# Optimization experiments

Hardware: AMD Instinct MI355X
Metric: run time of the kernel (lower is better)

The kernel has to match this reference:

```python
import jax, jax.numpy as jnp
import numpy as np

RES = (64, 128, 256)          # res_plane per scale
CDIM = (32, 32, 32)           # plane_feat_dim per scale
PADDING = 0.1
EPS = 1e-5                    # torch code uses 10e-6
PLANE_AXES = {"xz": (0, 2), "xy": (0, 1), "yz": (1, 2)}


def _plane_features(coord, feats, plane, res):
    """coord: (B,N,3) float, feats: (B,N,C) float -> (B,C,res,res).
    Faithful to normalize_coordinate + coordinate2index + scatter_mean."""
    a, b = PLANE_AXES[plane]
    xy = jnp.stack([coord[..., a], coord[..., b]], axis=-1)   # (B,N,2)
    xy = xy / (1.0 + PADDING + EPS) + 0.5
    xy = jnp.clip(xy, 0.0, 1.0 - EPS)
    ij = (xy * res).astype(jnp.int32)                         # trunc == floor (nonneg)
    idx = ij[..., 0] + res * ij[..., 1]                       # (B,N) flattened grid index
    r2 = res * res

    def per_batch(f, i):  # f: (N,C), i: (N,)
        s = jax.ops.segment_sum(f, i, num_segments=r2)        # (R2,C) scatter-add
        c = jax.ops.segment_sum(jnp.ones((f.shape[0],), f.dtype), i, num_segments=r2)
        return s / jnp.maximum(c, 1.0)[:, None]               # scatter_mean: div by clamp(count,1)

    out = jax.vmap(per_batch)(feats, idx)                     # (B,R2,C)
    B, _, C = out.shape
    return out.transpose(0, 2, 1).reshape(B, C, res, res)


def _forward(f_list, c_list):
    # returns tuple over 3 scales, each a tuple (xz, xy, yz) of (B,C,res,res)
    return tuple(
        tuple(_plane_features(c, f, pl, r) for pl in ("xz", "xy", "yz"))
        for f, c, r in zip(f_list, c_list, RES)
    )


def setup_inputs() -> dict:
    key = jax.random.key(0)
    ks = jax.random.split(key, 6)
    B = 8
    Ns = (65536, 32768, 16384)
    inp = {}
    for i, (n, c) in enumerate(zip(Ns, CDIM)):
        inp[f"f{i}"] = jax.random.normal(ks[i], (B, n, c), dtype=jnp.float32)
        # coords in [-0.5, 0.5): normalize maps them into [0,1) grid range
        inp[f"c{i}"] = jax.random.uniform(ks[3 + i], (B, n, 3), dtype=jnp.float32) - 0.5
    return inp


def reference(f0, f1, f2, c0, c1, c2):
    return _forward((f0, f1, f2), (c0, c1, c2))
```

## Files before the change

### kernel.cpp

```cpp
#include <hip/hip_runtime.h>

static constexpr int B = 8;
static constexpr int C = 32;

typedef float vfloat4 __attribute__((ext_vector_type(4)));

static constexpr size_t CNT0 = 0,        CNT1 = 98304,    CNT2 = 491520;
static constexpr size_t CNT_TOTAL = 2064384;
static constexpr size_t OFF0 = 2064384,  OFF1 = 2162688,  OFF2 = 2555904;
static constexpr size_t REC0 = 4128768,  REC1 = 5701632,  REC2 = 6488064;
static constexpr size_t LIST0 = 13762560, LIST1 = 15335424, LIST2 = 16121856;
static constexpr size_t OUT0 = 0, OUT1 = 3145728, OUT2 = 15728640;

__device__ __forceinline__ void plane_cells(float x, float y, float z, int res,
                                            int idxs[3])
{
#pragma clang fp contract(off)
    constexpr float denomf = (float)(1.0 + 0.1 + 1e-5);
    constexpr float recipf = 1.0f / denomf;
    constexpr float hi     = (float)(1.0 - 1e-5);
    const float rf = (float)res;
    const float tx = x * recipf;
    const float ty = y * recipf;
    const float tz = z * recipf;
    const float ux = fminf(fmaxf(tx + 0.5f, 0.0f), hi);
    const float uy = fminf(fmaxf(ty + 0.5f, 0.0f), hi);
    const float uz = fminf(fmaxf(tz + 0.5f, 0.0f), hi);
    const int ix = (int)(ux * rf);
    const int iy = (int)(uy * rf);
    const int iz = (int)(uz * rf);
    idxs[0] = ix + res * iz;
    idxs[1] = ix + res * iy;
    idxs[2] = iy + res * iz;
}

__global__ __launch_bounds__(256) void fused_count_rank(
    const float* __restrict__ c0, const float* __restrict__ c1,
    const float* __restrict__ c2, unsigned int* __restrict__ ws)
{
    int blk = blockIdx.x;
    const float* coords; int N, res; size_t cntB, recB;
    if (blk < 2048)      {              coords = c0; N = 65536; res = 64;  cntB = CNT0; recB = REC0; }
    else if (blk < 3072) { blk -= 2048; coords = c1; N = 32768; res = 128; cntB = CNT1; recB = REC1; }
    else                 { blk -= 3072; coords = c2; N = 16384; res = 256; cntB = CNT2; recB = REC2; }
    const int b = blk & 7;
    const int p = (blk >> 3) * 256 + threadIdx.x;
    const size_t pt = (size_t)b * N + p;
    const float x = coords[pt * 3 + 0];
    const float y = coords[pt * 3 + 1];
    const float z = coords[pt * 3 + 2];
    int idxs[3];
    plane_cells(x, y, z, res, idxs);
    const int R2 = res * res;
    unsigned int* cnt = ws + cntB;
    unsigned int* rec = ws + recB;
#pragma unroll
    for (int k = 0; k < 3; ++k) {
        const unsigned int cell = (unsigned int)idxs[k];
        const unsigned int rank =
            atomicAdd(&cnt[((size_t)k * B + b) * R2 + cell], 1u);
        rec[((size_t)k * B + b) * N + p] = (cell << 16) | rank;
    }
}

__global__ __launch_bounds__(1024) void fused_scan(unsigned int* __restrict__ ws)
{
    __shared__ unsigned int sdata[1024];
    int blk = blockIdx.x;
    size_t cntB, offB; int R2;
    if (blk < 24)      {              cntB = CNT0; offB = OFF0; R2 = 4096; }
    else if (blk < 48) { blk -= 24;   cntB = CNT1; offB = OFF1; R2 = 16384; }
    else               { blk -= 48;   cntB = CNT2; offB = OFF2; R2 = 65536; }
    const size_t base = (size_t)blk * (size_t)R2;
    const uint4* cnt4 = (const uint4*)(ws + cntB + base);
    uint4* off4 = (uint4*)(ws + offB + base);
    const int E4 = R2 >> 12;
    const int tid = threadIdx.x;
    unsigned int tsum = 0;
    for (int i = 0; i < E4; ++i) {
        const uint4 cc = cnt4[tid * E4 + i];
        tsum += cc.x + cc.y + cc.z + cc.w;
    }
    sdata[tid] = tsum;
    __syncthreads();
    for (int d = 1; d < 1024; d <<= 1) {
        unsigned int v = (tid >= d) ? sdata[tid - d] : 0u;
        __syncthreads();
        sdata[tid] += v;
        __syncthreads();
    }
    unsigned int run = sdata[tid] - tsum;
    for (int i = 0; i < E4; ++i) {
        const uint4 cc = cnt4[tid * E4 + i];
        uint4 o;
        o.x = run; run += cc.x;
        o.y = run; run += cc.y;
        o.z = run; run += cc.z;
        o.w = run; run += cc.w;
        off4[tid * E4 + i] = o;
    }
}

__global__ __launch_bounds__(256) void fused_build_list(unsigned int* __restrict__ ws)
{
    int blk = blockIdx.x;
    int N, R2; size_t recB, offB, listB;
    if (blk < 6144)      {              N = 65536; R2 = 4096;  recB = REC0; offB = OFF0; listB = LIST0; }
    else if (blk < 9216) { blk -= 6144; N = 32768; R2 = 16384; recB = REC1; offB = OFF1; listB = LIST1; }
    else                 { blk -= 9216; N = 16384; R2 = 65536; recB = REC2; offB = OFF2; listB = LIST2; }
    const int kb    = blk % 24;
    const int chunk = blk / 24;
    const int p = chunk * 256 + threadIdx.x;
    const unsigned int* rec = ws + recB;
    const unsigned int* off = ws + offB;
    unsigned short* list = (unsigned short*)ws + listB;
    const unsigned int r = rec[(size_t)kb * N + p];
    const unsigned int cell = r >> 16;
    const unsigned int rank = r & 0xffffu;
    const unsigned int pos = off[(size_t)kb * R2 + cell] + rank;
    list[(size_t)kb * N + pos] = (unsigned short)p;
}

__global__ __launch_bounds__(256) void fused_gather_mean(
    const float* __restrict__ f0, const float* __restrict__ f1,
    const float* __restrict__ f2, const unsigned int* __restrict__ ws,
    float* __restrict__ out)
{
    __shared__ float tile[C][64];
    __shared__ unsigned int s_cnt[64];
    __shared__ unsigned int s_off[64];
    int blk = blockIdx.x;
    const float* feats; int N, R2; size_t cntB, offB, listB, outB;
    if (blk < 1536)      {              feats = f0; N = 65536; R2 = 4096;  cntB = CNT0; offB = OFF0; listB = LIST0; outB = OUT0; }
    else if (blk < 7680) { blk -= 1536; feats = f1; N = 32768; R2 = 16384; cntB = CNT1; offB = OFF1; listB = LIST1; outB = OUT1; }
    else                 { blk -= 7680; feats = f2; N = 16384; R2 = 65536; cntB = CNT2; offB = OFF2; listB = LIST2; outB = OUT2; }
    const int kb       = blk % 24;
    const int cellBase = (blk / 24) * 64;
    const int b = kb & (B - 1);
    const int h   = threadIdx.x >> 5;
    const int sub = (threadIdx.x >> 3) & 3;
    const int chq = threadIdx.x & 7;
    const size_t segBase  = (size_t)kb * R2;
    const size_t listBase = (size_t)kb * N;
    const unsigned short* list = (const unsigned short*)ws + listB;
    const char* fB = (const char*)(feats + (size_t)b * N * C);
    const unsigned int laneOff = (unsigned int)chq << 4;

    if (threadIdx.x < 64) {
        s_cnt[threadIdx.x] = ws[cntB + segBase + cellBase + threadIdx.x];
        s_off[threadIdx.x] = ws[offB + segBase + cellBase + threadIdx.x];
    }
    __syncthreads();

    for (int i = 0; i < 8; ++i) {
        const int lc  = h * 8 + i;
        const int glc = lc >> 2, w = lc & 3;
        const int pcol = (((glc & 8) | ((glc & 7) ^ chq)) << 2) | w;
        const unsigned int n = s_cnt[lc];
        if (n == 0u) {
            if (sub == 0) {
                tile[chq * 4 + 0][pcol] = 0.0f;
                tile[chq * 4 + 1][pcol] = 0.0f;
                tile[chq * 4 + 2][pcol] = 0.0f;
                tile[chq * 4 + 3][pcol] = 0.0f;
            }
            continue;
        }
        const unsigned short* lp = list + listBase + s_off[lc];
        float ax = 0.0f, ay = 0.0f, az = 0.0f, aw = 0.0f;
        unsigned int j = 0;
        for (; j + 8 <= n; j += 8) {
            const unsigned int oA = ((unsigned int)lp[j + sub]     << 7) + laneOff;
            const unsigned int oB = ((unsigned int)lp[j + 4 + sub] << 7) + laneOff;
            const float4 vA = *(const float4*)(fB + oA);
            const float4 vB = *(const float4*)(fB + oB);
            ax += vA.x + vB.x; ay += vA.y + vB.y;
            az += vA.z + vB.z; aw += vA.w + vB.w;
        }
        if (j + sub < n) {
            const unsigned int o = ((unsigned int)lp[j + sub] << 7) + laneOff;
            const float4 v = *(const float4*)(fB + o);
            ax += v.x; ay += v.y; az += v.z; aw += v.w;
        }
        if (j + 4 + sub < n) {
            const unsigned int o = ((unsigned int)lp[j + 4 + sub] << 7) + laneOff;
            const float4 v = *(const float4*)(fB + o);
            ax += v.x; ay += v.y; az += v.z; aw += v.w;
        }
        ax += __shfl_xor(ax, 8);  ay += __shfl_xor(ay, 8);
        az += __shfl_xor(az, 8);  aw += __shfl_xor(aw, 8);
        ax += __shfl_xor(ax, 16); ay += __shfl_xor(ay, 16);
        az += __shfl_xor(az, 16); aw += __shfl_xor(aw, 16);
        if (sub == 0) {
            const float r = __builtin_amdgcn_rcpf((float)n);
            tile[chq * 4 + 0][pcol] = ax * r;
            tile[chq * 4 + 1][pcol] = ay * r;
            tile[chq * 4 + 2][pcol] = az * r;
            tile[chq * 4 + 3][pcol] = aw * r;
        }
    }
    __syncthreads();
    {
        const int ch2 = threadIdx.x >> 3;
        const int g   = threadIdx.x & 7;
        const int e   = ch2 >> 2;
        float* orow = out + outB + ((size_t)kb * C + ch2) * R2 + cellBase;
#pragma unroll
        for (int gg = 0; gg < 2; ++gg) {
            const int grp = g + gg * 8;
            const int pg  = (grp & 8) | ((grp & 7) ^ e);
            const vfloat4 v = *(const vfloat4*)&tile[ch2][pg * 4];
            __builtin_nontemporal_store(v, (vfloat4*)(orow + grp * 4));
        }
    }
}

extern "C" void kernel_launch(void* const* d_in, const int* in_sizes, int n_in,
                              void* d_out, int out_size, void* d_ws, size_t ws_size,
                              hipStream_t stream)
{
    const float *f[3], *c[3];
    const bool interleaved = in_sizes[1] < in_sizes[2];
    if (interleaved) {
        f[0] = (const float*)d_in[0]; c[0] = (const float*)d_in[1];
        f[1] = (const float*)d_in[2]; c[1] = (const float*)d_in[3];
        f[2] = (const float*)d_in[4]; c[2] = (const float*)d_in[5];
    } else {
        f[0] = (const float*)d_in[0]; f[1] = (const float*)d_in[1];
        f[2] = (const float*)d_in[2];
        c[0] = (const float*)d_in[3]; c[1] = (const float*)d_in[4];
        c[2] = (const float*)d_in[5];
    }

    unsigned int* ws32 = (unsigned int*)d_ws;
    float* out = (float*)d_out;

    hipMemsetAsync(d_ws, 0, CNT_TOTAL * sizeof(unsigned int), stream);

    fused_count_rank<<<dim3(3584), 256, 0, stream>>>(c[0], c[1], c[2], ws32);
    fused_scan<<<dim3(72), 1024, 0, stream>>>(ws32);
    fused_build_list<<<dim3(10752), 256, 0, stream>>>(ws32);
    fused_gather_mean<<<dim3(32256), 256, 0, stream>>>(f[0], f[1], f[2], ws32, out);
}
```

Baseline: 617.9 us.

## Recompute cells in list build and drop stored rank records

The counting pass no longer writes per-point cell/rank records. The list-building pass instead recomputes plane cells from the coordinates and takes slots with atomicAdd on the offset array, so each offset ends up as the segment end. The gather pass subtracts the count to find the segment start. This removes a large record write and read in exchange for a second round of atomics and a coordinate reload. Point order within a cell becomes nondeterministic, which can change float summation order slightly.

```diff
diff --git a/kernel.cpp b/kernel.cpp
--- a/kernel.cpp
+++ b/kernel.cpp
@@ -8,7 +8,6 @@
 static constexpr size_t CNT0 = 0,        CNT1 = 98304,    CNT2 = 491520;
 static constexpr size_t CNT_TOTAL = 2064384;
 static constexpr size_t OFF0 = 2064384,  OFF1 = 2162688,  OFF2 = 2555904;
-static constexpr size_t REC0 = 4128768,  REC1 = 5701632,  REC2 = 6488064;
 static constexpr size_t LIST0 = 13762560, LIST1 = 15335424, LIST2 = 16121856;
 static constexpr size_t OUT0 = 0, OUT1 = 3145728, OUT2 = 15728640;
 
@@ -39,10 +38,10 @@
     const float* __restrict__ c2, unsigned int* __restrict__ ws)
 {
     int blk = blockIdx.x;
-    const float* coords; int N, res; size_t cntB, recB;
-    if (blk < 2048)      {              coords = c0; N = 65536; res = 64;  cntB = CNT0; recB = REC0; }
-    else if (blk < 3072) { blk -= 2048; coords = c1; N = 32768; res = 128; cntB = CNT1; recB = REC1; }
-    else                 { blk -= 3072; coords = c2; N = 16384; res = 256; cntB = CNT2; recB = REC2; }
+    const float* coords; int N, res; size_t cntB;
+    if (blk < 2048)      {              coords = c0; N = 65536; res = 64;  cntB = CNT0; }
+    else if (blk < 3072) { blk -= 2048; coords = c1; N = 32768; res = 128; cntB = CNT1; }
+    else                 { blk -= 3072; coords = c2; N = 16384; res = 256; cntB = CNT2; }
     const int b = blk & 7;
     const int p = (blk >> 3) * 256 + threadIdx.x;
     const size_t pt = (size_t)b * N + p;
@@ -53,13 +52,9 @@
     plane_cells(x, y, z, res, idxs);
     const int R2 = res * res;
     unsigned int* cnt = ws + cntB;
-    unsigned int* rec = ws + recB;
 #pragma unroll
     for (int k = 0; k < 3; ++k) {
-        const unsigned int cell = (unsigned int)idxs[k];
-        const unsigned int rank =
-            atomicAdd(&cnt[((size_t)k * B + b) * R2 + cell], 1u);
-        rec[((size_t)k * B + b) * N + p] = (cell << 16) | rank;
+        atomicAdd(&cnt[((size_t)k * B + b) * R2 + (unsigned int)idxs[k]], 1u);
     }
 }
 
@@ -101,24 +96,32 @@
     }
 }
 
-__global__ __launch_bounds__(256) void fused_build_list(unsigned int* __restrict__ ws)
-{
-    int blk = blockIdx.x;
-    int N, R2; size_t recB, offB, listB;
-    if (blk < 6144)      {              N = 65536; R2 = 4096;  recB = REC0; offB = OFF0; listB = LIST0; }
-    else if (blk < 9216) { blk -= 6144; N = 32768; R2 = 16384; recB = REC1; offB = OFF1; listB = LIST1; }
-    else                 { blk -= 9216; N = 16384; R2 = 65536; recB = REC2; offB = OFF2; listB = LIST2; }
-    const int kb    = blk % 24;
-    const int chunk = blk / 24;
-    const int p = chunk * 256 + threadIdx.x;
-    const unsigned int* rec = ws + recB;
-    const unsigned int* off = ws + offB;
+__global__ __launch_bounds__(256) void fused_build_list(
+    const float* __restrict__ c0, const float* __restrict__ c1,
+    const float* __restrict__ c2, unsigned int* __restrict__ ws)
+{
+    int blk = blockIdx.x;
+    const float* coords; int N, res; size_t offB, listB;
+    if (blk < 2048)      {              coords = c0; N = 65536; res = 64;  offB = OFF0; listB = LIST0; }
+    else if (blk < 3072) { blk -= 2048; coords = c1; N = 32768; res = 128; offB = OFF1; listB = LIST1; }
+    else                 { blk -= 3072; coords = c2; N = 16384; res = 256; offB = OFF2; listB = LIST2; }
+    const int b = blk & 7;
+    const int p = (blk >> 3) * 256 + threadIdx.x;
+    const size_t pt = (size_t)b * N + p;
+    const float x = coords[pt * 3 + 0];
+    const float y = coords[pt * 3 + 1];
+    const float z = coords[pt * 3 + 2];
+    int idxs[3];
+    plane_cells(x, y, z, res, idxs);
+    const int R2 = res * res;
+    unsigned int* off = ws + offB;
     unsigned short* list = (unsigned short*)ws + listB;
-    const unsigned int r = rec[(size_t)kb * N + p];
-    const unsigned int cell = r >> 16;
-    const unsigned int rank = r & 0xffffu;
-    const unsigned int pos = off[(size_t)kb * R2 + cell] + rank;
-    list[(size_t)kb * N + pos] = (unsigned short)p;
+#pragma unroll
+    for (int k = 0; k < 3; ++k) {
+        const unsigned int pos =
+            atomicAdd(&off[((size_t)k * B + b) * R2 + (unsigned int)idxs[k]], 1u);
+        list[((size_t)k * B + b) * N + pos] = (unsigned short)p;
+    }
 }
 
 __global__ __launch_bounds__(256) void fused_gather_mean(
@@ -166,7 +169,7 @@
             }
             continue;
         }
-        const unsigned short* lp = list + listBase + s_off[lc];
+        const unsigned short* lp = list + listBase + (s_off[lc] - n);
         float ax = 0.0f, ay = 0.0f, az = 0.0f, aw = 0.0f;
         unsigned int j = 0;
         for (; j + 8 <= n; j += 8) {
@@ -239,6 +242,6 @@
 
     fused_count_rank<<<dim3(3584), 256, 0, stream>>>(c[0], c[1], c[2], ws32);
     fused_scan<<<dim3(72), 1024, 0, stream>>>(ws32);
-    fused_build_list<<<dim3(10752), 256, 0, stream>>>(ws32);
+    fused_build_list<<<dim3(3584), 256, 0, stream>>>(c[0], c[1], c[2], ws32);
     fused_gather_mean<<<dim3(32256), 256, 0, stream>>>(f[0], f[1], f[2], ws32, out);
 }
```

After: 702.7 us. 1.14x slower.
